# Kernel optimization log

Hardware: AMD Instinct MI355X
Metric: run time of the kernel (lower is better)

## Reference

```python
import jax, jax.numpy as jnp
import numpy as np

D_MODEL, N_HEADS, D_FF = 1024, 16, 4096
SCALE = 0.1          # lookup-activation input quantization step
NUM_BITS = 8
LEVELS = 1 << NUM_BITS   # 256
HALF = LEVELS // 2       # 128
MAX_EXP = 4
EPS = 1e-5


def pow2_weight(key, shape, max_exp=MAX_EXP):
    """Ternary power-of-two weights: values in {0, +/-2^{-e}}, e in [max_exp, max_exp+3].
    Exponent range keeps fan-in-1024 outputs O(1)."""
    k1, k2 = jax.random.split(key)
    sign = jax.random.randint(k1, shape, -1, 2).astype(jnp.float32)  # {-1,0,1}
    e = jax.random.randint(k2, shape, max_exp, max_exp + 4).astype(jnp.float32)
    return sign * jnp.exp2(-e)


def setup_inputs() -> dict:
    key = jax.random.key(0)
    ks = jax.random.split(key, 8)
    x = jax.random.normal(ks[0], (4, 2048, D_MODEL), dtype=jnp.float32)
    return {
        "x": x,
        "ln1_g": jnp.ones((D_MODEL,), jnp.float32),
        "ln1_b": jnp.zeros((D_MODEL,), jnp.float32),
        "wq": pow2_weight(ks[1], (D_MODEL, D_MODEL)),
        "wk": pow2_weight(ks[2], (D_MODEL, D_MODEL)),
        "wv": pow2_weight(ks[3], (D_MODEL, D_MODEL)),
        "wo": pow2_weight(ks[4], (D_MODEL, D_MODEL)),
        "ln2_g": jnp.ones((D_MODEL,), jnp.float32),
        "ln2_b": jnp.zeros((D_MODEL,), jnp.float32),
        "w1": pow2_weight(ks[5], (D_MODEL, D_FF)),
        "w2": pow2_weight(ks[6], (D_FF, D_MODEL)),
    }


def _layernorm(x, g, b):
    mu = jnp.mean(x, axis=-1, keepdims=True)
    var = jnp.var(x, axis=-1, keepdims=True)
    return (x - mu) * jax.lax.rsqrt(var + EPS) * g + b


def _lookup_act(x):
    # StructuredLookupActivation: quantize input to 2^num_bits levels, gather from
    # a precomputed GELU table (proved via Lasso lookup in the SNARK).
    grid = (jnp.arange(LEVELS, dtype=jnp.float32) - HALF) * SCALE
    table = jax.nn.gelu(grid)
    idx = jnp.clip(jnp.round(x / SCALE).astype(jnp.int32) + HALF, 0, LEVELS - 1)
    return table[idx]


def _linear_attention(x, wq, wk, wv, wo):
    B, S, D = x.shape
    H, Dh = N_HEADS, D // N_HEADS
    q = (x @ wq).reshape(B, S, H, Dh)
    k = (x @ wk).reshape(B, S, H, Dh)
    v = (x @ wv).reshape(B, S, H, Dh)
    # elu+1 feature map -> O(S*Dh^2) linear attention (no [S,S] scores)
    phi_q = jax.nn.elu(q) + 1.0
    phi_k = jax.nn.elu(k) + 1.0
    kv = jnp.einsum('bshd,bshe->bhde', phi_k, v)          # [B,H,Dh,Dh]
    z = jnp.sum(phi_k, axis=1)                            # [B,H,Dh]
    num = jnp.einsum('bshd,bhde->bshe', phi_q, kv)        # [B,S,H,Dh]
    den = jnp.einsum('bshd,bhd->bsh', phi_q, z)[..., None] + 1e-6
    out = (num / den).reshape(B, S, D)
    return out @ wo


def reference(x, ln1_g, ln1_b, wq, wk, wv, wo, ln2_g, ln2_b, w1, w2):
    # norm -> linear attention -> residual
    x = x + _linear_attention(_layernorm(x, ln1_g, ln1_b), wq, wk, wv, wo)
    # norm -> ternary FFN with lookup activation -> residual
    h = _layernorm(x, ln2_g, ln2_b)
    x = x + (_lookup_act(h @ w1) @ w2)
    return x
```

## Files before the change

kernel.cpp:

```cpp
#include <hip/hip_runtime.h>
#include <cstdint>
#include <cstddef>


#define D_MODEL 1024
#define SEQ     2048
#define BATCH   4
#define NTOK    8192
#define NHEADS  16
#define DH      64
#define DFF     4096
#define KVCH    16
#define CHROWS  (SEQ / KVCH)
#define PSTRIDE 4160

typedef _Float16 half8 __attribute__((ext_vector_type(8)));
typedef float f32x4 __attribute__((ext_vector_type(4)));
typedef unsigned int u32x4 __attribute__((ext_vector_type(4)));

__device__ __forceinline__ unsigned short f2h(float x) {
  _Float16 h = (_Float16)x;
  union { _Float16 h; unsigned short u; } c; c.h = h; return c.u;
}
__device__ __forceinline__ float h2f(unsigned short u) {
  union { unsigned short u; _Float16 h; } c; c.u = u; return (float)c.h;
}

__device__ __forceinline__ float phi_act(float x) {
  return x > 0.f ? x + 1.f : expf(x);
}

__device__ __forceinline__ float gelu_exact(float v) {
  float c = 0.7978845608028654f;
  float t = tanhf(c * (v + 0.044715f * v * v * v));
  return 0.5f * v * (1.f + t);
}

__device__ __forceinline__ void gl_lds16(const void* g, void* l) {
  __builtin_amdgcn_global_load_lds(
      (const __attribute__((address_space(1))) unsigned int*)g,
      (__attribute__((address_space(3))) unsigned int*)l, 16, 0, 0);
}

__device__ __forceinline__ void convT_body(const float* __restrict__ W,
                                           unsigned short* __restrict__ WT,
                                           int K, int N, int bx, int by, int t) {
  __shared__ float tile[64][65];
  int kb = by << 6, nb = bx << 6;
  int rr = t >> 4, cc = (t & 15) << 2;
#pragma unroll
  for (int i = 0; i < 4; ++i) {
    int r = rr + (i << 4);
    float4 v = *(const float4*)(W + (size_t)(kb + r) * N + nb + cc);
    tile[r][cc] = v.x; tile[r][cc + 1] = v.y; tile[r][cc + 2] = v.z; tile[r][cc + 3] = v.w;
  }
  __syncthreads();
#pragma unroll
  for (int i = 0; i < 4; ++i) {
    int n = rr + (i << 4);
    ushort4 o;
    o.x = f2h(tile[cc + 0][n]); o.y = f2h(tile[cc + 1][n]);
    o.z = f2h(tile[cc + 2][n]); o.w = f2h(tile[cc + 3][n]);
    *(ushort4*)(WT + (size_t)(nb + n) * K + kb + cc) = o;
  }
}

__device__ __forceinline__ void ln_body(const float* __restrict__ X,
                                        const float* __restrict__ g,
                                        const float* __restrict__ b,
                                        unsigned short* __restrict__ Y,
                                        int tok, int t) {
  const float4* xr = (const float4*)(X + (size_t)tok * D_MODEL);
  float4 v = xr[t];
  float s  = v.x + v.y + v.z + v.w;
  float s2 = v.x * v.x + v.y * v.y + v.z * v.z + v.w * v.w;
#pragma unroll
  for (int o = 32; o > 0; o >>= 1) {
    s  += __shfl_down(s, o);
    s2 += __shfl_down(s2, o);
  }
  __shared__ float red[8];
  __shared__ float mu_s, rs_s;
  int wid = t >> 6;
  if ((t & 63) == 0) { red[wid] = s; red[wid + 4] = s2; }
  __syncthreads();
  if (t == 0) {
    float ts  = red[0] + red[1] + red[2] + red[3];
    float ts2 = red[4] + red[5] + red[6] + red[7];
    float mu  = ts * (1.f / D_MODEL);
    float var = ts2 * (1.f / D_MODEL) - mu * mu;
    mu_s = mu;
    rs_s = rsqrtf(var + 1e-5f);
  }
  __syncthreads();
  float mu = mu_s, rs = rs_s;
  float4 gv = ((const float4*)g)[t];
  float4 bv = ((const float4*)b)[t];
  ushort4 hv;
  hv.x = f2h((v.x - mu) * rs * gv.x + bv.x);
  hv.y = f2h((v.y - mu) * rs * gv.y + bv.y);
  hv.z = f2h((v.z - mu) * rs * gv.z + bv.z);
  hv.w = f2h((v.w - mu) * rs * gv.w + bv.w);
  ((ushort4*)(Y + (size_t)tok * D_MODEL))[t] = hv;
}

__global__ __launch_bounds__(256) void prep_kernel(
    const float* __restrict__ wq, const float* __restrict__ wk,
    const float* __restrict__ wv, const float* __restrict__ wo,
    const float* __restrict__ w1, const float* __restrict__ w2,
    const float* __restrict__ x, const float* __restrict__ g,
    const float* __restrict__ b,
    unsigned short* __restrict__ wqkvT, unsigned short* __restrict__ woT,
    unsigned short* __restrict__ w1T, unsigned short* __restrict__ w2T,
    unsigned short* __restrict__ xn) {
  int f = blockIdx.x;
  int t = threadIdx.x;
  if (f < 1024) {
    int job = f >> 8, r = f & 255;
    const float* W = (job == 0) ? wq : (job == 1) ? wk : (job == 2) ? wv : wo;
    unsigned short* D = (job == 3) ? woT
                                   : wqkvT + (size_t)job * D_MODEL * D_MODEL;
    convT_body(W, D, D_MODEL, D_MODEL, r & 15, r >> 4, t);
  } else if (f < 2048) {
    int r = f - 1024;
    convT_body(w1, w1T, D_MODEL, DFF, r & 63, r >> 6, t);
  } else if (f < 3072) {
    int r = f - 2048;
    convT_body(w2, w2T, DFF, D_MODEL, r & 15, r >> 4, t);
  } else {
    ln_body(x, g, b, xn, f - 3072, t);
  }
}

__global__ __launch_bounds__(256) void ln_kernel(const float* __restrict__ X,
                                                 const float* __restrict__ g,
                                                 const float* __restrict__ b,
                                                 unsigned short* __restrict__ Y) {
  ln_body(X, g, b, Y, blockIdx.x, threadIdx.x);
}

template <int EP, int BK>
__global__ __launch_bounds__(256, (BK == 64) ? 4 : 2) void mfma_gemm(
    const unsigned short* __restrict__ A,
    const unsigned short* __restrict__ BT,
    void* Cv, const float* R, int N, int K) {
  constexpr int SEGS = BK / 8;
  constexpr int RPC  = 64 / SEGS;
  constexpr int NJ   = 32 / RPC;
  __shared__ unsigned short smem[2 * 128 * BK];
  __shared__ float gtab[EP == 3 ? 256 : 1];
  unsigned short* sA = smem;
  unsigned short* sB = smem + 128 * BK;

  int t = threadIdx.x;
  if (EP == 3) gtab[t & 255] = gelu_exact((float)((t & 255) - 128) * 0.1f);

  int bm, bn;
  {
    int L = blockIdx.y * gridDim.x + blockIdx.x;
    if ((gridDim.y & 7) == 0) {
      int xcd = L & 7, wi = L >> 3;
      int mPerX = gridDim.y >> 3;
      bm = xcd * mPerX + wi / gridDim.x;
      bn = wi % gridDim.x;
    } else {
      bn = blockIdx.x; bm = blockIdx.y;
    }
  }

  int w = t >> 6, l = t & 63;
  int lrow = l / SEGS;
  int lseg = l & (SEGS - 1);
  int m0 = bm << 7;
  int n0 = bn << 7;
  size_t strideB = (size_t)K * 2;

  const char* gA[NJ]; const char* gB[NJ];
  int ldsOff[NJ];
#pragma unroll
  for (int j = 0; j < NJ; ++j) {
    int row = (w << 5) + j * RPC + lrow;
    int gso = (lseg ^ (row & 7)) << 4;
    gA[j] = (const char*)A + (size_t)(m0 + row) * strideB + gso;
    gB[j] = (const char*)BT + (size_t)(n0 + row) * strideB + gso;
    ldsOff[j] = ((w << 5) + j * RPC) * BK;
  }

  int wm = w >> 1, wn = w & 1;
  int m16 = l & 15, qd = l >> 4;

  f32x4 acc[4][4];
#pragma unroll
  for (int i = 0; i < 4; ++i)
#pragma unroll
    for (int j = 0; j < 4; ++j) acc[i][j] = (f32x4){0.f, 0.f, 0.f, 0.f};

  for (int k0 = 0; k0 < K; k0 += BK) {
    size_t kb = (size_t)k0 * 2;
#pragma unroll
    for (int j = 0; j < NJ; ++j) {
      gl_lds16(gA[j] + kb, sA + ldsOff[j]);
      gl_lds16(gB[j] + kb, sB + ldsOff[j]);
    }
    __syncthreads();
#pragma unroll
    for (int kk = 0; kk < BK / 32; ++kk) {
      int ksb = (kk << 2) + qd;
      half8 af[4], bf[4];
#pragma unroll
      for (int mt = 0; mt < 4; ++mt) {
        int r = (wm << 6) + (mt << 4) + m16;
        int slot = ksb ^ (r & 7);
        af[mt] = *(const half8*)(sA + r * BK + (slot << 3));
      }
#pragma unroll
      for (int nt = 0; nt < 4; ++nt) {
        int r = (wn << 6) + (nt << 4) + m16;
        int slot = ksb ^ (r & 7);
        bf[nt] = *(const half8*)(sB + r * BK + (slot << 3));
      }
#pragma unroll
      for (int mt = 0; mt < 4; ++mt)
#pragma unroll
        for (int nt = 0; nt < 4; ++nt)
          acc[mt][nt] = __builtin_amdgcn_mfma_f32_16x16x32_f16(af[mt], bf[nt], acc[mt][nt], 0, 0, 0);
    }
    __syncthreads();
  }

  int sel = n0 >> 10;
  size_t slab = (size_t)sel * ((size_t)NTOK * D_MODEL);
  int colL = (n0 & 1023) + (wn << 6) + m16;

  int colBase = n0 + (wn << 6) + m16;
#pragma unroll
  for (int mt = 0; mt < 4; ++mt) {
    int rBase = m0 + (wm << 6) + (mt << 4) + (qd << 2);
#pragma unroll
    for (int nt = 0; nt < 4; ++nt) {
      int col = colBase + (nt << 4);
#pragma unroll
      for (int i = 0; i < 4; ++i) {
        float v = acc[mt][nt][i];
        if (EP == 4) {
          if (sel < 2) v = phi_act(v);
          size_t idx = slab + (size_t)(rBase + i) * D_MODEL + colL + (nt << 4);
          ((unsigned short*)Cv)[idx] = f2h(v);
        } else {
          size_t idx = (size_t)(rBase + i) * N + col;
          if (EP == 2)      ((float*)Cv)[idx] = R[idx] + v;
          else if (EP == 3) {
            float r = rintf(v / 0.1f);
            int iq = (int)r + 128;
            iq = iq < 0 ? 0 : (iq > 255 ? 255 : iq);
            ((unsigned short*)Cv)[idx] = f2h(gtab[iq]);
          } else          ((float*)Cv)[idx] = v;
        }
      }
    }
  }
}

__global__ __launch_bounds__(256) void kvz_partial(const unsigned short* __restrict__ PK,
                                                   const unsigned short* __restrict__ V,
                                                   float* __restrict__ P) {
  int c = blockIdx.x, bh = blockIdx.y;
  int b = bh >> 4, h = bh & 15;
  __shared__ float pk[8][64];
  __shared__ float vv[8][64];
  int t = threadIdx.x;
  const size_t base = ((size_t)b * SEQ + (size_t)c * CHROWS) * D_MODEL + h * DH;
  int u = t & 127;
  int lrow = u >> 4;
  int lcol = (u & 15) << 2;
  bool isV = (t >= 128);
  const unsigned short* src = isV ? V : PK;
  int dkb = (t >> 4) << 2;
  int deb = (t & 15) << 2;
  float acc[4][4] = {};
  float zacc = 0.f;
  for (int s0 = 0; s0 < CHROWS; s0 += 8) {
    ushort4 ld = *(const ushort4*)(src + base + (size_t)(s0 + lrow) * D_MODEL + lcol);
    float f0 = h2f(ld.x), f1 = h2f(ld.y), f2 = h2f(ld.z), f3 = h2f(ld.w);
    __syncthreads();
    if (isV) { vv[lrow][lcol] = f0; vv[lrow][lcol+1] = f1; vv[lrow][lcol+2] = f2; vv[lrow][lcol+3] = f3; }
    else     { pk[lrow][lcol] = f0; pk[lrow][lcol+1] = f1; pk[lrow][lcol+2] = f2; pk[lrow][lcol+3] = f3; }
    __syncthreads();
#pragma unroll
    for (int ss = 0; ss < 8; ++ss) {
      float4 a  = *(const float4*)&pk[ss][dkb];
      float4 bb = *(const float4*)&vv[ss][deb];
      acc[0][0] += a.x * bb.x; acc[0][1] += a.x * bb.y; acc[0][2] += a.x * bb.z; acc[0][3] += a.x * bb.w;
      acc[1][0] += a.y * bb.x; acc[1][1] += a.y * bb.y; acc[1][2] += a.y * bb.z; acc[1][3] += a.y * bb.w;
      acc[2][0] += a.z * bb.x; acc[2][1] += a.z * bb.y; acc[2][2] += a.z * bb.z; acc[2][3] += a.z * bb.w;
      acc[3][0] += a.w * bb.x; acc[3][1] += a.w * bb.y; acc[3][2] += a.w * bb.z; acc[3][3] += a.w * bb.w;
    }
    if (t < 64) {
#pragma unroll
      for (int ss = 0; ss < 8; ++ss) zacc += pk[ss][t];
    }
  }
  float* Pb = P + ((size_t)c * 64 + bh) * PSTRIDE;
#pragma unroll
  for (int i = 0; i < 4; ++i) {
    float4 o; o.x = acc[i][0]; o.y = acc[i][1]; o.z = acc[i][2]; o.w = acc[i][3];
    *(float4*)(Pb + (size_t)(dkb + i) * DH + deb) = o;
  }
  if (t < 64) Pb[4096 + t] = zacc;
}

__global__ __launch_bounds__(256) void kvz_reduce(const float* __restrict__ P,
                                                  unsigned short* __restrict__ KVT,
                                                  float* __restrict__ Z) {
  int bh = blockIdx.x;
  int q = blockIdx.y;
  int t = threadIdx.x;
  int lo = q * (PSTRIDE / 4), hi = lo + (PSTRIDE / 4);
  for (int i = lo + t; i < hi; i += 256) {
    float s = 0.f;
#pragma unroll
    for (int c = 0; c < KVCH; ++c)
      s += P[((size_t)c * 64 + bh) * PSTRIDE + i];
    if (i < 4096) {
      int d = i >> 6, e = i & 63;
      KVT[(size_t)bh * 4096 + e * 64 + d] = f2h(s);
    } else {
      Z[(size_t)bh * 64 + (i - 4096)] = s;
    }
  }
}

__global__ __launch_bounds__(256) void attn_mfma(const unsigned short* __restrict__ PQ,
                                                 const unsigned short* __restrict__ KVT,
                                                 const float* __restrict__ Z,
                                                 unsigned short* __restrict__ O) {
  __shared__ unsigned short sA[256 * 64];
  __shared__ unsigned short sB[64 * 64];
  __shared__ float zsh[64];
  __shared__ float dsh[256];
  int t = threadIdx.x;
  int tok0 = blockIdx.x << 8;
  int h = blockIdx.y;
  int b = tok0 >> 11;
  int bh = b * NHEADS + h;

  const unsigned short* aSrc = PQ + (size_t)tok0 * D_MODEL + h * DH;
#pragma unroll
  for (int j = 0; j < 8; ++j) {
    int id = t + (j << 8);
    int r = id >> 3, s = id & 7;
    u32x4 v = *(const u32x4*)(aSrc + (size_t)r * D_MODEL + (s << 3));
    *(u32x4*)(sA + r * 64 + ((s ^ (r & 7)) << 3)) = v;
  }
  const unsigned short* bSrc = KVT + (size_t)bh * 4096;
#pragma unroll
  for (int j = 0; j < 2; ++j) {
    int id = t + (j << 8);
    int r = id >> 3, s = id & 7;
    u32x4 v = *(const u32x4*)(bSrc + r * 64 + (s << 3));
    *(u32x4*)(sB + r * 64 + ((s ^ (r & 7)) << 3)) = v;
  }
  if (t < 64) zsh[t] = Z[(size_t)bh * 64 + t];
  __syncthreads();

  {
    float d_ = 1e-6f;
#pragma unroll
    for (int s = 0; s < 8; ++s) {
      half8 q = *(const half8*)(sA + t * 64 + (((s ^ (t & 7))) << 3));
#pragma unroll
      for (int j = 0; j < 8; ++j)
        d_ += (float)q[j] * zsh[(s << 3) + j];
    }
    dsh[t] = d_;
  }

  int w = t >> 6, l = t & 63;
  int m16 = l & 15, qd = l >> 4;
  int wrow = w << 6;

  f32x4 acc[4][4];
#pragma unroll
  for (int i = 0; i < 4; ++i)
#pragma unroll
    for (int j = 0; j < 4; ++j) acc[i][j] = (f32x4){0.f, 0.f, 0.f, 0.f};

#pragma unroll
  for (int kk = 0; kk < 2; ++kk) {
    int ksb = (kk << 2) + qd;
    half8 af[4], bf[4];
#pragma unroll
    for (int mt = 0; mt < 4; ++mt) {
      int r = wrow + (mt << 4) + m16;
      af[mt] = *(const half8*)(sA + r * 64 + ((ksb ^ (r & 7)) << 3));
    }
#pragma unroll
    for (int nt = 0; nt < 4; ++nt) {
      int r = (nt << 4) + m16;
      bf[nt] = *(const half8*)(sB + r * 64 + ((ksb ^ (r & 7)) << 3));
    }
#pragma unroll
    for (int mt = 0; mt < 4; ++mt)
#pragma unroll
      for (int nt = 0; nt < 4; ++nt)
        acc[mt][nt] = __builtin_amdgcn_mfma_f32_16x16x32_f16(af[mt], bf[nt], acc[mt][nt], 0, 0, 0);
  }
  __syncthreads();

#pragma unroll
  for (int mt = 0; mt < 4; ++mt) {
#pragma unroll
    for (int i = 0; i < 4; ++i) {
      int rloc = wrow + (mt << 4) + (qd << 2) + i;
      float rcp = 1.f / dsh[rloc];
      size_t obase = (size_t)(tok0 + rloc) * D_MODEL + h * DH + m16;
#pragma unroll
      for (int nt = 0; nt < 4; ++nt)
        O[obase + (nt << 4)] = f2h(acc[mt][nt][i] * rcp);
    }
  }
}

extern "C" void kernel_launch(void* const* d_in, const int* in_sizes, int n_in,
                              void* d_out, int out_size, void* d_ws, size_t ws_size,
                              hipStream_t stream) {
  const float* x    = (const float*)d_in[0];
  const float* ln1g = (const float*)d_in[1];
  const float* ln1b = (const float*)d_in[2];
  const float* wq   = (const float*)d_in[3];
  const float* wk   = (const float*)d_in[4];
  const float* wv   = (const float*)d_in[5];
  const float* wo   = (const float*)d_in[6];
  const float* ln2g = (const float*)d_in[7];
  const float* ln2b = (const float*)d_in[8];
  const float* w1   = (const float*)d_in[9];
  const float* w2   = (const float*)d_in[10];
  float* out = (float*)d_out;
  char* ws = (char*)d_ws;

  const size_t MB = 1024 * 1024;
  unsigned short* xn   = (unsigned short*)(ws);
  unsigned short* qkv  = (unsigned short*)(ws + 32 * MB);
  unsigned short* phiq = qkv;
  unsigned short* phik = qkv + (size_t)NTOK * D_MODEL;
  unsigned short* vbuf = qkv + 2 * (size_t)NTOK * D_MODEL;
  unsigned short* ffn  = (unsigned short*)(ws + 32 * MB);
  unsigned short* w1T  = (unsigned short*)(ws + 96 * MB);
  unsigned short* w2T  = (unsigned short*)(ws + 104 * MB);
  unsigned short* woT  = (unsigned short*)(ws + 128 * MB);

  unsigned short* wqkvT = (unsigned short*)d_out;
  float* kvP = (float*)((char*)d_out + 6 * MB);
  unsigned short* kvT16 = (unsigned short*)((char*)d_out + 24 * MB);
  float* z   = (float*)((char*)d_out + 25 * MB);

  dim3 blk(256);

  prep_kernel<<<dim3(3072 + NTOK), blk, 0, stream>>>(
      wq, wk, wv, wo, w1, w2, x, ln1g, ln1b, wqkvT, woT, w1T, w2T, xn);

  dim3 gQKV(3 * D_MODEL / 128, NTOK / 128);
  mfma_gemm<4, 64><<<gQKV, blk, 0, stream>>>(xn, wqkvT, qkv, nullptr, 3 * D_MODEL, D_MODEL);

  kvz_partial<<<dim3(KVCH, BATCH * NHEADS), blk, 0, stream>>>(phik, vbuf, kvP);
  kvz_reduce<<<dim3(BATCH * NHEADS, 4), blk, 0, stream>>>(kvP, kvT16, z);

  attn_mfma<<<dim3(NTOK / 256, NHEADS), blk, 0, stream>>>(phiq, kvT16, z, xn);

  dim3 gD(D_MODEL / 128, NTOK / 128);
  mfma_gemm<2, 128><<<gD, blk, 0, stream>>>(xn, woT, out, x, D_MODEL, D_MODEL);

  ln_kernel<<<NTOK, blk, 0, stream>>>(out, ln2g, ln2b, xn);

  dim3 gF(DFF / 128, NTOK / 128);
  mfma_gemm<3, 64><<<gF, blk, 0, stream>>>(xn, w1T, ffn, nullptr, DFF, D_MODEL);

  mfma_gemm<2, 128><<<gD, blk, 0, stream>>>(ffn, w2T, out, out, D_MODEL, DFF);
}
```

Baseline: 438.8 us.

## Add 256x128-tile GEMM for QKV and FFN1, halve KV chunk count

Adds a new GEMM kernel with 256x128 output tiles, where each wave computes a 128x64 sub-tile with 8x4 MFMA accumulators. It is used for the QKV projection (with phi epilogue) and the FFN up-projection (with the lookup-GELU epilogue), to raise arithmetic intensity and reuse of the B operand per LDS load. The generic GEMM keeps only the plain epilogues. KV partial chunking also drops from 16 to 8 chunks per sequence, which means fewer partials to reduce but less parallelism. The larger accumulator footprint raises register pressure, and launch bounds of 2 blocks per CU may limit occupancy.

Measured after the change: 428.6 us (median of 2 runs). 1.02x faster.

```diff
diff --git a/kernel.cpp b/kernel.cpp
--- a/kernel.cpp
+++ b/kernel.cpp
@@ -10,7 +10,7 @@
 #define NHEADS  16
 #define DH      64
 #define DFF     4096
-#define KVCH    16
+#define KVCH    8
 #define CHROWS  (SEQ / KVCH)
 #define PSTRIDE 4160
 
@@ -228,17 +228,119 @@
     __syncthreads();
   }
 
+  int colBase = n0 + (wn << 6) + m16;
+#pragma unroll
+  for (int mt = 0; mt < 4; ++mt) {
+    int rBase = m0 + (wm << 6) + (mt << 4) + (qd << 2);
+#pragma unroll
+    for (int nt = 0; nt < 4; ++nt) {
+      int col = colBase + (nt << 4);
+#pragma unroll
+      for (int i = 0; i < 4; ++i) {
+        float v = acc[mt][nt][i];
+        size_t idx = (size_t)(rBase + i) * N + col;
+        if (EP == 2)      ((float*)Cv)[idx] = R[idx] + v;
+        else if (EP == 3) {
+          float r = rintf(v / 0.1f);
+          int iq = (int)r + 128;
+          iq = iq < 0 ? 0 : (iq > 255 ? 255 : iq);
+          ((unsigned short*)Cv)[idx] = f2h(gtab[iq]);
+        } else          ((float*)Cv)[idx] = v;
+      }
+    }
+  }
+}
+
+template <int EP>
+__global__ __launch_bounds__(256, 2) void mfma_gemm_fat(
+    const unsigned short* __restrict__ A,
+    const unsigned short* __restrict__ BT,
+    void* Cv, int N, int K) {
+  constexpr int BK = 64;
+  __shared__ unsigned short sA[256 * BK];
+  __shared__ unsigned short sB[128 * BK];
+  __shared__ float gtab[EP == 3 ? 256 : 1];
+
+  int t = threadIdx.x;
+  if (EP == 3) gtab[t & 255] = gelu_exact((float)((t & 255) - 128) * 0.1f);
+
+  int bm, bn;
+  {
+    int L = blockIdx.y * gridDim.x + blockIdx.x;
+    if ((gridDim.y & 7) == 0) {
+      int xcd = L & 7, wi = L >> 3;
+      int mPerX = gridDim.y >> 3;
+      bm = xcd * mPerX + wi / gridDim.x;
+      bn = wi % gridDim.x;
+    } else {
+      bn = blockIdx.x; bm = blockIdx.y;
+    }
+  }
+  int m0 = bm << 8, n0 = bn << 7;
+
+  int w = t >> 6, l = t & 63;
+  int lrow = l >> 3;
+  int lseg = l & 7;
+  size_t strideB = (size_t)K * 2;
+  size_t rstep8 = (size_t)8 * strideB;
+
+  int rowA0 = (w << 6) + lrow;
+  int rowB0 = (w << 5) + lrow;
+  const char* gA0 = (const char*)A  + (size_t)(m0 + rowA0) * strideB + ((lseg ^ (rowA0 & 7)) << 4);
+  const char* gB0 = (const char*)BT + (size_t)(n0 + rowB0) * strideB + ((lseg ^ (rowB0 & 7)) << 4);
+  int ldsA0 = ((w << 6)) * BK;
+  int ldsB0 = ((w << 5)) * BK;
+
+  int wm = w >> 1, wn = w & 1;
+  int m16 = l & 15, qd = l >> 4;
+
+  f32x4 acc[8][4];
+#pragma unroll
+  for (int i = 0; i < 8; ++i)
+#pragma unroll
+    for (int j = 0; j < 4; ++j) acc[i][j] = (f32x4){0.f, 0.f, 0.f, 0.f};
+
+  for (int k0 = 0; k0 < K; k0 += BK) {
+    size_t kb = (size_t)k0 * 2;
+#pragma unroll
+    for (int j = 0; j < 8; ++j)
+      gl_lds16(gA0 + kb + j * rstep8, sA + ldsA0 + j * 512);
+#pragma unroll
+    for (int j = 0; j < 4; ++j)
+      gl_lds16(gB0 + kb + j * rstep8, sB + ldsB0 + j * 512);
+    __syncthreads();
+#pragma unroll
+    for (int kk = 0; kk < 2; ++kk) {
+      int ksb = (kk << 2) + qd;
+      half8 af[8], bf[4];
+#pragma unroll
+      for (int mt = 0; mt < 8; ++mt) {
+        int r = (wm << 7) + (mt << 4) + m16;
+        af[mt] = *(const half8*)(sA + r * BK + ((ksb ^ (r & 7)) << 3));
+      }
+#pragma unroll
+      for (int nt = 0; nt < 4; ++nt) {
+        int r = (wn << 6) + (nt << 4) + m16;
+        bf[nt] = *(const half8*)(sB + r * BK + ((ksb ^ (r & 7)) << 3));
+      }
+#pragma unroll
+      for (int mt = 0; mt < 8; ++mt)
+#pragma unroll
+        for (int nt = 0; nt < 4; ++nt)
+          acc[mt][nt] = __builtin_amdgcn_mfma_f32_16x16x32_f16(af[mt], bf[nt], acc[mt][nt], 0, 0, 0);
+    }
+    __syncthreads();
+  }
+
   int sel = n0 >> 10;
   size_t slab = (size_t)sel * ((size_t)NTOK * D_MODEL);
   int colL = (n0 & 1023) + (wn << 6) + m16;
-
   int colBase = n0 + (wn << 6) + m16;
 #pragma unroll
-  for (int mt = 0; mt < 4; ++mt) {
-    int rBase = m0 + (wm << 6) + (mt << 4) + (qd << 2);
+  for (int mt = 0; mt < 8; ++mt) {
+    int rBase = m0 + (wm << 7) + (mt << 4) + (qd << 2);
 #pragma unroll
     for (int nt = 0; nt < 4; ++nt) {
-      int col = colBase + (nt << 4);
 #pragma unroll
       for (int i = 0; i < 4; ++i) {
         float v = acc[mt][nt][i];
@@ -247,14 +349,10 @@
           size_t idx = slab + (size_t)(rBase + i) * D_MODEL + colL + (nt << 4);
           ((unsigned short*)Cv)[idx] = f2h(v);
         } else {
-          size_t idx = (size_t)(rBase + i) * N + col;
-          if (EP == 2)      ((float*)Cv)[idx] = R[idx] + v;
-          else if (EP == 3) {
-            float r = rintf(v / 0.1f);
-            int iq = (int)r + 128;
-            iq = iq < 0 ? 0 : (iq > 255 ? 255 : iq);
-            ((unsigned short*)Cv)[idx] = f2h(gtab[iq]);
-          } else          ((float*)Cv)[idx] = v;
+          float r = rintf(v / 0.1f);
+          int iq = (int)r + 128;
+          iq = iq < 0 ? 0 : (iq > 255 ? 255 : iq);
+          ((unsigned short*)Cv)[(size_t)(rBase + i) * N + colBase + (nt << 4)] = f2h(gtab[iq]);
         }
       }
     }
@@ -459,8 +557,8 @@
   prep_kernel<<<dim3(3072 + NTOK), blk, 0, stream>>>(
       wq, wk, wv, wo, w1, w2, x, ln1g, ln1b, wqkvT, woT, w1T, w2T, xn);
 
-  dim3 gQKV(3 * D_MODEL / 128, NTOK / 128);
-  mfma_gemm<4, 64><<<gQKV, blk, 0, stream>>>(xn, wqkvT, qkv, nullptr, 3 * D_MODEL, D_MODEL);
+  dim3 gQKV(3 * D_MODEL / 128, NTOK / 256);
+  mfma_gemm_fat<4><<<gQKV, blk, 0, stream>>>(xn, wqkvT, qkv, 3 * D_MODEL, D_MODEL);
 
   kvz_partial<<<dim3(KVCH, BATCH * NHEADS), blk, 0, stream>>>(phik, vbuf, kvP);
   kvz_reduce<<<dim3(BATCH * NHEADS, 4), blk, 0, stream>>>(kvP, kvT16, z);
@@ -472,8 +570,8 @@
 
   ln_kernel<<<NTOK, blk, 0, stream>>>(out, ln2g, ln2b, xn);
 
-  dim3 gF(DFF / 128, NTOK / 128);
-  mfma_gemm<3, 64><<<gF, blk, 0, stream>>>(xn, w1T, ffn, nullptr, DFF, D_MODEL);
+  dim3 gF(DFF / 128, NTOK / 256);
+  mfma_gemm_fat<3><<<gF, blk, 0, stream>>>(xn, w1T, ffn, DFF, D_MODEL);
 
   mfma_gemm<2, 128><<<gD, blk, 0, stream>>>(ffn, w2T, out, out, D_MODEL, DFF);
 }
```
